# Kernel tuning notes

Hardware: AMD Instinct MI355X
Metric: run time of the kernel (lower is better)

## Reference

```python
import jax, jax.numpy as jnp
import numpy as np

K = 3        # ksize
S = 2        # stride_1
P = K // 2   # padding
SCALE = 10.0 # softmax_scale


def conv1x1(x, w, bias):
    # x: [bs, C, D, H, W], w: [O, C] (1x1x1 Conv3d), bias: [O]
    return jnp.einsum('bcdhw,oc->bodhw', x, w) + bias[None, :, None, None, None]


def _win_idx(n_in):
    n_out = (n_in + 2 * P - K) // S + 1
    idx = (jnp.arange(n_out) * S)[:, None] + jnp.arange(K)  # [n_out, K]
    return idx, n_out


def unfold2d(x):
    # x: [bs, C, H, W] -> patches [bs, C, nH, nW, K, K] (torch Unfold semantics, zero pad)
    bs, C, H, W = x.shape
    xp = jnp.pad(x, ((0, 0), (0, 0), (P, P), (P, P)))
    ri, nH = _win_idx(H)
    ci, nW = _win_idx(W)
    return xp[:, :, ri[:, None, :, None], ci[None, :, None, :]]


def fold2d(pat, H, W):
    # pat: [bs, C, nH, nW, K, K] -> [bs, C, H, W] via overlap-add (torch Fold)
    bs, C, nH, nW, _, _ = pat.shape
    ri, _ = _win_idx(H)
    ci, _ = _win_idx(W)
    out = jnp.zeros((bs, C, H + 2 * P, W + 2 * P), pat.dtype)
    out = out.at[:, :, ri[:, None, :, None], ci[None, :, None, :]].add(pat)
    return out[:, :, P:P + H, P:P + W]


def _patches_flat(x2d):
    # x2d: [bs, Ci, H, W] -> ([bs*L, Ci*K*K], nH, nW)  matching torch's
    # unfold -> view(bs,Ci,K,K,L) -> permute(0,4,1,2,3) -> reshape layout
    pat = unfold2d(x2d)                      # [bs, Ci, nH, nW, K, K]
    bs, Ci, nH, nW = pat.shape[:4]
    flat = jnp.transpose(pat, (0, 2, 3, 1, 4, 5)).reshape(bs * nH * nW, Ci * K * K)
    return flat, nH, nW


def salsa_one(b_one, g_w, g_b, th_w, th_b, ph_w, ph_b, W_w, W_b):
    bs, C, D, H, W = b_one.shape
    Ci = g_w.shape[0]
    b1 = conv1x1(b_one, g_w, g_b)    # query source
    b2 = conv1x1(b_one, th_w, th_b)  # value source
    b3 = conv1x1(b_one, ph_w, ph_b)  # key source
    mid = D // 2

    q, nH, nW = _patches_flat(b1[:, :, mid])   # [bs*L, Ci*K*K]
    v, _, _ = _patches_flat(b2[:, :, mid])
    kq, _, _ = _patches_flat(b3[:, :, mid])

    att = jax.nn.softmax(SCALE * (q @ kq.T), axis=1)  # [bs*L, bs*L]
    zi = att @ v                                      # [bs*L, Ci*K*K]

    pat = jnp.transpose(zi.reshape(bs, nH, nW, Ci, K, K), (0, 3, 1, 2, 4, 5))
    zi2 = fold2d(pat, H, W)                           # [bs, Ci, H, W]
    # overlap-count normalization: fold(unfold(ones))
    mask = fold2d(unfold2d(jnp.ones((bs, Ci, H, W), b_one.dtype)), H, W)
    zi2 = zi2 / mask

    zi5 = jnp.broadcast_to(zi2[:, :, None], (bs, Ci, D, H, W))
    return b_one + conv1x1(zi5, W_w, W_b)


def setup_inputs() -> dict:
    key = jax.random.key(0)
    ks = jax.random.split(key, 9)
    C, Ci = 64, 16
    b = jax.random.normal(ks[0], (2, 1, C, 8, 160, 160), dtype=jnp.float32)
    mk = lambda k, shp: jax.random.normal(k, shp, dtype=jnp.float32) * 0.05
    return {
        'b': b,
        'g_w': mk(ks[1], (Ci, C)), 'g_b': mk(ks[2], (Ci,)),
        'theta_w': mk(ks[3], (Ci, C)), 'theta_b': mk(ks[4], (Ci,)),
        'phi_w': mk(ks[5], (Ci, C)), 'phi_b': mk(ks[6], (Ci,)),
        'W_w': mk(ks[7], (C, Ci)), 'W_b': mk(ks[8], (C,)),
    }


def reference(b, g_w, g_b, theta_w, theta_b, phi_w, phi_b, W_w, W_b):
    f = lambda x: salsa_one(x, g_w, g_b, theta_w, theta_b, phi_w, phi_b, W_w, W_b)
    return jax.vmap(f)(b)
```

## Files before the change

### kernel.cpp

```cpp
#include <hip/hip_runtime.h>


#define NPIX 25600
#define LOG2E10 14.42695040888963f
#define TAU 0.75f

typedef float floatx16 __attribute__((ext_vector_type(16)));
typedef short short8 __attribute__((ext_vector_type(8)));

__device__ inline unsigned short f2bf(float x) {
    union { float f; unsigned int u; } v; v.f = x;
    unsigned int r = v.u + 0x7fffu + ((v.u >> 16) & 1u);
    return (unsigned short)(r >> 16);
}
__device__ inline float bf2f(unsigned short u) {
    union { unsigned int u; float f; } v; v.u = ((unsigned int)u) << 16;
    return v.f;
}

__global__ void k_proj(const float* __restrict__ b,
                       const float* __restrict__ gw, const float* __restrict__ gb,
                       const float* __restrict__ thw, const float* __restrict__ thb,
                       const float* __restrict__ phw, const float* __restrict__ phb,
                       float* __restrict__ P3) {
    __shared__ float Wl[3 * 1024];
    __shared__ float Bl[48];
    int tid = threadIdx.x;
    int g = blockIdx.y;
    int pix = blockIdx.x * 256 + tid;
    for (int i = tid; i < 1024; i += 256) {
        Wl[i]        = gw[i];
        Wl[1024 + i] = phw[i];
        Wl[2048 + i] = thw[i];
    }
    if (tid < 16) { Bl[tid] = gb[tid]; Bl[16 + tid] = phb[tid]; Bl[32 + tid] = thb[tid]; }
    __syncthreads();

    float acc[48];
#pragma unroll
    for (int o = 0; o < 48; o++) acc[o] = 0.f;
    const float* bp = b + (size_t)g * 64 * 8 * NPIX + (size_t)4 * NPIX + pix;
    for (int c = 0; c < 64; c++) {
        float xv = bp[(size_t)c * 8 * NPIX];
#pragma unroll
        for (int o = 0; o < 48; o++)
            acc[o] += Wl[(o >> 4) * 1024 + (o & 15) * 64 + c] * xv;
    }
#pragma unroll
    for (int o = 0; o < 48; o++)
        P3[(size_t)(g * 48 + o) * NPIX + pix] = acc[o] + Bl[o];
}

__global__ void k_unfold_qk(const float* __restrict__ P3, unsigned short* __restrict__ Pat) {
    int idx = blockIdx.x * 256 + threadIdx.x;
    int f = idx % 144;
    int l = (idx / 144) % 6400;
    int s = (idx / (144 * 6400)) & 1;
    int g = idx / (2 * 144 * 6400);
    int ci = f / 9, kr = (f % 9) / 3, kc = f % 3;
    int oh = l / 80, ow = l % 80;
    int h = oh * 2 + kr - 1, w = ow * 2 + kc - 1;
    float v = 0.f;
    if (h >= 0 && h < 160 && w >= 0 && w < 160)
        v = P3[(size_t)(g * 48 + s * 16 + ci) * NPIX + h * 160 + w];
    Pat[idx] = f2bf(v);
}

__global__ void k_unfold_v(const float* __restrict__ P3, unsigned short* __restrict__ VT) {
    int idx = blockIdx.x * 256 + threadIdx.x;
    int l = idx % 6400;
    int f = (idx / 6400) % 144;
    int g = idx / (144 * 6400);
    int ci = f / 9, kr = (f % 9) / 3, kc = f % 3;
    int oh = l / 80, ow = l % 80;
    int h = oh * 2 + kr - 1, w = ow * 2 + kc - 1;
    float v = 0.f;
    if (h >= 0 && h < 160 && w >= 0 && w < 160)
        v = P3[(size_t)(g * 48 + 32 + ci) * NPIX + h * 160 + w];
    VT[idx] = f2bf(v);
}

__global__ __launch_bounds__(256, 2) void k_attn(
    const unsigned short* __restrict__ PatQK, const unsigned short* __restrict__ VT,
    float* __restrict__ ml, unsigned short* __restrict__ Opart,
    int nsplit, int kps) {
    __shared__ unsigned short Ks[64 * 156];
    __shared__ unsigned short Vs[160 * 76];
    __shared__ unsigned short Pl[4 * 32 * 76];

    int tid = threadIdx.x;
    int lane = tid & 63;
    int w = tid >> 6;
    int l31 = lane & 31;
    int h5 = lane >> 5;
    int split = blockIdx.y, g = blockIdx.z;
    int q = blockIdx.x * 128 + w * 32 + l31;
    int nIter = kps >> 6;

    const unsigned short* Qg = PatQK + ((size_t)g * 2 + 0) * 6400 * 144;
    const unsigned short* Kg = PatQK + ((size_t)g * 2 + 1) * 6400 * 144 + (size_t)split * kps * 144;
    const unsigned short* Vg = VT + (size_t)g * 144 * 6400 + split * kps;

    short8 qf[9];
#pragma unroll
    for (int fs = 0; fs < 9; fs++)
        qf[fs] = *(const short8*)(Qg + (size_t)q * 144 + fs * 16 + h5 * 8);

    floatx16 O[5];
#pragma unroll
    for (int i = 0; i < 5; i++) O[i] = (floatx16)0.f;
    float m = -1e30f, lsum = 0.f;

    unsigned short* Plw = Pl + w * (32 * 76);

    short8 stg[9];
    {
#pragma unroll
        for (int j = 0; j < 9; j++) {
            int c = tid + 256 * j;
            if (c < 1152) {
                int row = c / 18, col = c - row * 18;
                stg[j] = *(const short8*)(Kg + row * 144 + col * 8);
            } else {
                int vv = c - 1152;
                int f = vv >> 3, col = vv & 7;
                stg[j] = *(const short8*)(Vg + (size_t)f * 6400 + col * 8);
            }
        }
#pragma unroll
        for (int j = 0; j < 9; j++) {
            int c = tid + 256 * j;
            if (c < 1152) {
                int row = c / 18, col = c - row * 18;
                *(short8*)&Ks[row * 156 + col * 8] = stg[j];
            } else {
                int vv = c - 1152;
                int f = vv >> 3, col = vv & 7;
                *(short8*)&Vs[f * 76 + col * 8] = stg[j];
            }
        }
    }

    for (int it = 0; it < nIter; it++) {
        __syncthreads();

        if (it + 1 < nIter) {
            const unsigned short* Kt = Kg + (it + 1) * 64 * 144;
            const unsigned short* Vt = Vg + (it + 1) * 64;
#pragma unroll
            for (int j = 0; j < 9; j++) {
                int c = tid + 256 * j;
                if (c < 1152) {
                    int row = c / 18, col = c - row * 18;
                    stg[j] = *(const short8*)(Kt + row * 144 + col * 8);
                } else {
                    int vv = c - 1152;
                    int f = vv >> 3, col = vv & 7;
                    stg[j] = *(const short8*)(Vt + (size_t)f * 6400 + col * 8);
                }
            }
        }

        floatx16 S0 = (floatx16)0.f, S1 = (floatx16)0.f;
#pragma unroll
        for (int fs = 0; fs < 9; fs++) {
            short8 a0 = *(const short8*)&Ks[l31 * 156 + fs * 16 + h5 * 8];
            short8 a1 = *(const short8*)&Ks[(32 + l31) * 156 + fs * 16 + h5 * 8];
            S0 = __builtin_amdgcn_mfma_f32_32x32x16_bf16(a0, qf[fs], S0, 0, 0, 0);
            S1 = __builtin_amdgcn_mfma_f32_32x32x16_bf16(a1, qf[fs], S1, 0, 0, 0);
        }

        float mt = -1e30f;
#pragma unroll
        for (int r = 0; r < 16; r++) { mt = fmaxf(mt, S0[r]); mt = fmaxf(mt, S1[r]); }
        mt = fmaxf(mt, __shfl_xor(mt, 32, 64));
        bool upd = mt > m + TAU;
        float mnew = upd ? mt : m;
        float alpha = upd ? exp2f(LOG2E10 * (m - mnew)) : 1.f;
        float ps = 0.f;
#pragma unroll
        for (int r = 0; r < 16; r++) {
            S0[r] = exp2f(LOG2E10 * (S0[r] - mnew));
            S1[r] = exp2f(LOG2E10 * (S1[r] - mnew));
            ps += S0[r] + S1[r];
        }
        ps += __shfl_xor(ps, 32, 64);
        lsum = lsum * alpha + ps;
        m = mnew;
        if (__any(alpha < 1.f)) {
#pragma unroll
            for (int t5 = 0; t5 < 5; t5++)
#pragma unroll
                for (int r = 0; r < 16; r++) O[t5][r] *= alpha;
        }

#pragma unroll
        for (int rg = 0; rg < 4; rg++) {
            ushort4 w0, w1;
            w0.x = f2bf(S0[4 * rg + 0]); w0.y = f2bf(S0[4 * rg + 1]);
            w0.z = f2bf(S0[4 * rg + 2]); w0.w = f2bf(S0[4 * rg + 3]);
            w1.x = f2bf(S1[4 * rg + 0]); w1.y = f2bf(S1[4 * rg + 1]);
            w1.z = f2bf(S1[4 * rg + 2]); w1.w = f2bf(S1[4 * rg + 3]);
            *(ushort4*)&Plw[l31 * 76 + rg * 8 + h5 * 4] = w0;
            *(ushort4*)&Plw[l31 * 76 + 32 + rg * 8 + h5 * 4] = w1;
        }

#pragma unroll
        for (int ks = 0; ks < 4; ks++) {
            short8 pb = *(const short8*)&Plw[l31 * 76 + ks * 16 + h5 * 8];
#pragma unroll
            for (int ft = 0; ft < 5; ft++) {
                short8 va = *(const short8*)&Vs[(ft * 32 + l31) * 76 + ks * 16 + h5 * 8];
                O[ft] = __builtin_amdgcn_mfma_f32_32x32x16_bf16(va, pb, O[ft], 0, 0, 0);
            }
        }

        __syncthreads();
        if (it + 1 < nIter) {
#pragma unroll
            for (int j = 0; j < 9; j++) {
                int c = tid + 256 * j;
                if (c < 1152) {
                    int row = c / 18, col = c - row * 18;
                    *(short8*)&Ks[row * 156 + col * 8] = stg[j];
                } else {
                    int vv = c - 1152;
                    int f = vv >> 3, col = vv & 7;
                    *(short8*)&Vs[f * 76 + col * 8] = stg[j];
                }
            }
        }
    }

    if (h5 == 0)
        ((float2*)ml)[((size_t)g * nsplit + split) * 6400 + q] = make_float2(m, lsum);

    unsigned short* Og = Opart + (((size_t)g * nsplit + split) * 6400 + q) * 144;
#pragma unroll
    for (int ft = 0; ft < 5; ft++)
#pragma unroll
        for (int rg = 0; rg < 4; rg++) {
            int f = ft * 32 + rg * 8 + h5 * 4;
            if (f < 144) {
                ushort4 st;
                st.x = f2bf(O[ft][4 * rg + 0]); st.y = f2bf(O[ft][4 * rg + 1]);
                st.z = f2bf(O[ft][4 * rg + 2]); st.w = f2bf(O[ft][4 * rg + 3]);
                *(ushort4*)(Og + f) = st;
            }
        }
}

__global__ void k_merge(const float* __restrict__ mlp, const unsigned short* __restrict__ Opart,
                        float* __restrict__ Zi, int nsplit) {
    int idx = blockIdx.x * 256 + threadIdx.x;
    int fg = idx % 36;
    int q = (idx / 36) % 6400;
    int g = idx / (36 * 6400);
    const float2* ml2 = (const float2*)mlp;
    float2 s[5];
    float ms = -1e30f;
#pragma unroll
    for (int k = 0; k < 5; k++) {
        s[k] = (k < nsplit) ? ml2[((size_t)g * nsplit + k) * 6400 + q]
                            : make_float2(-1e30f, 0.f);
        ms = fmaxf(ms, s[k].x);
    }
    float wgt[5], denom = 0.f;
#pragma unroll
    for (int k = 0; k < 5; k++) {
        wgt[k] = exp2f(LOG2E10 * (s[k].x - ms));
        denom += wgt[k] * s[k].y;
    }
    float inv = 1.f / denom;
    float a0 = 0.f, a1 = 0.f, a2 = 0.f, a3 = 0.f;
#pragma unroll
    for (int k = 0; k < 5; k++) {
        if (k < nsplit) {
            ushort4 u = *(const ushort4*)(Opart + (((size_t)g * nsplit + k) * 6400 + q) * 144 + fg * 4);
            a0 += wgt[k] * bf2f(u.x); a1 += wgt[k] * bf2f(u.y);
            a2 += wgt[k] * bf2f(u.z); a3 += wgt[k] * bf2f(u.w);
        }
    }
    float4 out = make_float4(a0 * inv, a1 * inv, a2 * inv, a3 * inv);
    *(float4*)(Zi + ((size_t)g * 6400 + q) * 144 + fg * 4) = out;
}

__global__ void k_fold(const float* __restrict__ Zi, float* __restrict__ zi2) {
    int idx = blockIdx.x * 256 + threadIdx.x;
    int pix = idx % NPIX;
    int ci = (idx / NPIX) & 15;
    int g = idx / (16 * NPIX);
    int h = pix / 160, w = pix % 160;
    int ohs[2], krs[2], nh = 0;
#pragma unroll
    for (int kr = 0; kr < 3; kr++) {
        int t = h + 1 - kr;
        if (t >= 0 && (t & 1) == 0 && (t >> 1) < 80) { ohs[nh] = t >> 1; krs[nh] = kr; nh++; }
    }
    int ows[2], kcs[2], nw = 0;
#pragma unroll
    for (int kc = 0; kc < 3; kc++) {
        int t = w + 1 - kc;
        if (t >= 0 && (t & 1) == 0 && (t >> 1) < 80) { ows[nw] = t >> 1; kcs[nw] = kc; nw++; }
    }
    float sm = 0.f;
    for (int a = 0; a < nh; a++)
        for (int bb = 0; bb < nw; bb++) {
            int l = ohs[a] * 80 + ows[bb];
            int f = ci * 9 + krs[a] * 3 + kcs[bb];
            sm += Zi[((size_t)g * 6400 + l) * 144 + f];
        }
    zi2[idx] = sm / (float)(nh * nw);
}

__global__ void k_final(const float* __restrict__ b, const float* __restrict__ zi2,
                        const float* __restrict__ Ww, const float* __restrict__ Wb,
                        float* __restrict__ out) {
    __shared__ float z[16 * 64];
    __shared__ float Wl[64 * 16];
    __shared__ float Bl[64];
    int tid = threadIdx.x;
    int g = blockIdx.y;
    int pxb = blockIdx.x * 64;
    for (int i = tid; i < 1024; i += 256) {
        int ci = i >> 6, px = i & 63;
        z[i] = zi2[(size_t)(g * 16 + ci) * NPIX + pxb + px];
        Wl[i] = Ww[i];
    }
    if (tid < 64) Bl[tid] = Wb[tid];
    __syncthreads();

    int px4 = tid & 15;
    int cg = tid >> 4;
    float acc[4][4];
#pragma unroll
    for (int c4 = 0; c4 < 4; c4++) {
        float bv = Bl[cg + 16 * c4];
#pragma unroll
        for (int j = 0; j < 4; j++) acc[c4][j] = bv;
    }
#pragma unroll
    for (int ci = 0; ci < 16; ci++) {
        float zv[4];
#pragma unroll
        for (int j = 0; j < 4; j++) zv[j] = z[ci * 64 + px4 * 4 + j];
#pragma unroll
        for (int c4 = 0; c4 < 4; c4++) {
            float wv = Wl[(cg + 16 * c4) * 16 + ci];
#pragma unroll
            for (int j = 0; j < 4; j++) acc[c4][j] += wv * zv[j];
        }
    }
    for (int d = 0; d < 8; d++) {
#pragma unroll
        for (int c4 = 0; c4 < 4; c4++) {
            int c = cg + 16 * c4;
            size_t base = ((size_t)(g * 64 + c) * 8 + d) * NPIX + pxb + px4 * 4;
            float4 bv = *(const float4*)(b + base);
            float4 ov = make_float4(bv.x + acc[c4][0], bv.y + acc[c4][1],
                                    bv.z + acc[c4][2], bv.w + acc[c4][3]);
            *(float4*)(out + base) = ov;
        }
    }
}

extern "C" void kernel_launch(void* const* d_in, const int* in_sizes, int n_in,
                              void* d_out, int out_size, void* d_ws, size_t ws_size,
                              hipStream_t stream) {
    const float* b   = (const float*)d_in[0];
    const float* gw  = (const float*)d_in[1];
    const float* gb  = (const float*)d_in[2];
    const float* thw = (const float*)d_in[3];
    const float* thb = (const float*)d_in[4];
    const float* phw = (const float*)d_in[5];
    const float* phb = (const float*)d_in[6];
    const float* Ww  = (const float*)d_in[7];
    const float* Wb  = (const float*)d_in[8];
    float* out = (float*)d_out;
    float* ws = (float*)d_ws;

    const size_t need5 = 30003200;
    int ns = (ws_size >= need5) ? 5 : 4;
    int kps = 6400 / ns;

    unsigned short* PatQK = (unsigned short*)ws;
    unsigned short* VT    = (unsigned short*)(ws + 1843200);
    float*          ml    = ws + 2764800;
    size_t off_P3 = 2764800 + (size_t)2 * ns * 6400 * 2;
    float*          P3    = ws + off_P3;
    unsigned short* Opart = (unsigned short*)(ws + off_P3);
    float*          Zi    = ws;
    float*          zi2   = ws + 1843200;

    k_proj<<<dim3(100, 2), 256, 0, stream>>>(b, gw, gb, thw, thb, phw, phb, P3);
    k_unfold_qk<<<dim3(14400), 256, 0, stream>>>(P3, PatQK);
    k_unfold_v<<<dim3(7200), 256, 0, stream>>>(P3, VT);
    k_attn<<<dim3(50, ns, 2), 256, 0, stream>>>(PatQK, VT, ml, Opart, ns, kps);
    k_merge<<<dim3(1800), 256, 0, stream>>>(ml, Opart, Zi, ns);
    k_fold<<<dim3(3200), 256, 0, stream>>>(Zi, zi2);
    k_final<<<dim3(400, 2), 256, 0, stream>>>(b, zi2, Ww, Wb, out);
}
```

Measured before the change: 399.6 us.

## Keep softmax probabilities in registers and split projection channels across waves

```diff
diff --git a/kernel.cpp b/kernel.cpp
--- a/kernel.cpp
+++ b/kernel.cpp
@@ -7,6 +7,8 @@
 
 typedef float floatx16 __attribute__((ext_vector_type(16)));
 typedef short short8 __attribute__((ext_vector_type(8)));
+
+union U8 { short8 s8; unsigned int u[4]; };
 
 __device__ inline unsigned short f2bf(float x) {
     union { float f; unsigned int u; } v; v.f = x;
@@ -17,21 +19,35 @@
     union { unsigned int u; float f; } v; v.u = ((unsigned int)u) << 16;
     return v.f;
 }
-
-__global__ void k_proj(const float* __restrict__ b,
-                       const float* __restrict__ gw, const float* __restrict__ gb,
-                       const float* __restrict__ thw, const float* __restrict__ thb,
-                       const float* __restrict__ phw, const float* __restrict__ phb,
-                       float* __restrict__ P3) {
-    __shared__ float Wl[3 * 1024];
+__device__ inline unsigned int cvtpk(float a, float b) {
+    unsigned int r;
+    asm("v_cvt_pk_bf16_f32 %0, %1, %2" : "=v"(r) : "v"(a), "v"(b));
+    return r;
+}
+__device__ inline void perm32swap(unsigned int& a, unsigned int& b) {
+    asm("v_permlane32_swap_b32 %0, %1" : "+v"(a), "+v"(b));
+}
+
+__global__ __launch_bounds__(256) void k_proj(
+    const float* __restrict__ b,
+    const float* __restrict__ gw, const float* __restrict__ gb,
+    const float* __restrict__ thw, const float* __restrict__ thb,
+    const float* __restrict__ phw, const float* __restrict__ phb,
+    float* __restrict__ P3) {
+    __shared__ float Wt[3 * 64 * 16];
     __shared__ float Bl[48];
+    __shared__ float red[2][48][64];
     int tid = threadIdx.x;
     int g = blockIdx.y;
-    int pix = blockIdx.x * 256 + tid;
+    int px = tid & 63;
+    int cq = tid >> 6;
+    int pix = blockIdx.x * 64 + px;
+
     for (int i = tid; i < 1024; i += 256) {
-        Wl[i]        = gw[i];
-        Wl[1024 + i] = phw[i];
-        Wl[2048 + i] = thw[i];
+        int o = i & 15, c = i >> 4;
+        Wt[(0 * 64 + c) * 16 + o] = gw[o * 64 + c];
+        Wt[(1 * 64 + c) * 16 + o] = phw[o * 64 + c];
+        Wt[(2 * 64 + c) * 16 + o] = thw[o * 64 + c];
     }
     if (tid < 16) { Bl[tid] = gb[tid]; Bl[16 + tid] = phb[tid]; Bl[32 + tid] = thb[tid]; }
     __syncthreads();
@@ -40,15 +56,38 @@
 #pragma unroll
     for (int o = 0; o < 48; o++) acc[o] = 0.f;
     const float* bp = b + (size_t)g * 64 * 8 * NPIX + (size_t)4 * NPIX + pix;
-    for (int c = 0; c < 64; c++) {
+#pragma unroll
+    for (int i = 0; i < 16; i++) {
+        int c = cq * 16 + i;
         float xv = bp[(size_t)c * 8 * NPIX];
 #pragma unroll
+        for (int s = 0; s < 3; s++) {
+            const float* wp = &Wt[(s * 64 + c) * 16];
+#pragma unroll
+            for (int o = 0; o < 16; o++)
+                acc[s * 16 + o] += wp[o] * xv;
+        }
+    }
+    if (cq >= 2) {
+#pragma unroll
+        for (int o = 0; o < 48; o++) red[cq - 2][o][px] = acc[o];
+    }
+    __syncthreads();
+    if (cq < 2) {
+#pragma unroll
+        for (int o = 0; o < 48; o++) acc[o] += red[cq][o][px];
+    }
+    __syncthreads();
+    if (cq == 1) {
+#pragma unroll
+        for (int o = 0; o < 48; o++) red[0][o][px] = acc[o];
+    }
+    __syncthreads();
+    if (cq == 0) {
+#pragma unroll
         for (int o = 0; o < 48; o++)
-            acc[o] += Wl[(o >> 4) * 1024 + (o & 15) * 64 + c] * xv;
-    }
-#pragma unroll
-    for (int o = 0; o < 48; o++)
-        P3[(size_t)(g * 48 + o) * NPIX + pix] = acc[o] + Bl[o];
+            P3[(size_t)(g * 48 + o) * NPIX + pix] = acc[o] + red[0][o][px] + Bl[o];
+    }
 }
 
 __global__ void k_unfold_qk(const float* __restrict__ P3, unsigned short* __restrict__ Pat) {
@@ -84,9 +123,9 @@
     const unsigned short* __restrict__ PatQK, const unsigned short* __restrict__ VT,
     float* __restrict__ ml, unsigned short* __restrict__ Opart,
     int nsplit, int kps) {
-    __shared__ unsigned short Ks[64 * 156];
-    __shared__ unsigned short Vs[160 * 76];
-    __shared__ unsigned short Pl[4 * 32 * 76];
+    __shared__ unsigned short SM[64 * 156 + 160 * 76];
+    unsigned short* Ks = SM;
+    unsigned short* Vs = SM + 64 * 156;
 
     int tid = threadIdx.x;
     int lane = tid & 63;
@@ -111,57 +150,41 @@
     for (int i = 0; i < 5; i++) O[i] = (floatx16)0.f;
     float m = -1e30f, lsum = 0.f;
 
-    unsigned short* Plw = Pl + w * (32 * 76);
-
+    const unsigned short* gptr[9];
+    int gstep[9], loff[9];
+#pragma unroll
+    for (int j = 0; j < 9; j++) {
+        int c = tid + 256 * j;
+        if (c < 1152) {
+            int row = c / 18, col = c - row * 18;
+            gptr[j] = Kg + row * 144 + col * 8;
+            gstep[j] = 64 * 144;
+            loff[j] = (row * 156 + col * 8) * 2;
+        } else {
+            int vv = c - 1152;
+            int f = vv >> 3, col = vv & 7;
+            gptr[j] = Vg + (size_t)f * 6400 + col * 8;
+            gstep[j] = 64;
+            loff[j] = (64 * 156 + f * 76 + col * 8) * 2;
+        }
+    }
+    char* smb = (char*)SM;
     short8 stg[9];
-    {
-#pragma unroll
-        for (int j = 0; j < 9; j++) {
-            int c = tid + 256 * j;
-            if (c < 1152) {
-                int row = c / 18, col = c - row * 18;
-                stg[j] = *(const short8*)(Kg + row * 144 + col * 8);
-            } else {
-                int vv = c - 1152;
-                int f = vv >> 3, col = vv & 7;
-                stg[j] = *(const short8*)(Vg + (size_t)f * 6400 + col * 8);
-            }
-        }
-#pragma unroll
-        for (int j = 0; j < 9; j++) {
-            int c = tid + 256 * j;
-            if (c < 1152) {
-                int row = c / 18, col = c - row * 18;
-                *(short8*)&Ks[row * 156 + col * 8] = stg[j];
-            } else {
-                int vv = c - 1152;
-                int f = vv >> 3, col = vv & 7;
-                *(short8*)&Vs[f * 76 + col * 8] = stg[j];
-            }
-        }
-    }
+#pragma unroll
+    for (int j = 0; j < 9; j++) { stg[j] = *(const short8*)gptr[j]; gptr[j] += gstep[j]; }
+#pragma unroll
+    for (int j = 0; j < 9; j++) *(short8*)(smb + loff[j]) = stg[j];
 
     for (int it = 0; it < nIter; it++) {
         __syncthreads();
 
         if (it + 1 < nIter) {
-            const unsigned short* Kt = Kg + (it + 1) * 64 * 144;
-            const unsigned short* Vt = Vg + (it + 1) * 64;
-#pragma unroll
-            for (int j = 0; j < 9; j++) {
-                int c = tid + 256 * j;
-                if (c < 1152) {
-                    int row = c / 18, col = c - row * 18;
-                    stg[j] = *(const short8*)(Kt + row * 144 + col * 8);
-                } else {
-                    int vv = c - 1152;
-                    int f = vv >> 3, col = vv & 7;
-                    stg[j] = *(const short8*)(Vt + (size_t)f * 6400 + col * 8);
-                }
-            }
+#pragma unroll
+            for (int j = 0; j < 9; j++) { stg[j] = *(const short8*)gptr[j]; gptr[j] += gstep[j]; }
         }
 
         floatx16 S0 = (floatx16)0.f, S1 = (floatx16)0.f;
+        __builtin_amdgcn_s_setprio(1);
 #pragma unroll
         for (int fs = 0; fs < 9; fs++) {
             short8 a0 = *(const short8*)&Ks[l31 * 156 + fs * 16 + h5 * 8];
@@ -169,21 +192,32 @@
             S0 = __builtin_amdgcn_mfma_f32_32x32x16_bf16(a0, qf[fs], S0, 0, 0, 0);
             S1 = __builtin_amdgcn_mfma_f32_32x32x16_bf16(a1, qf[fs], S1, 0, 0, 0);
         }
-
-        float mt = -1e30f;
-#pragma unroll
-        for (int r = 0; r < 16; r++) { mt = fmaxf(mt, S0[r]); mt = fmaxf(mt, S1[r]); }
+        __builtin_amdgcn_s_setprio(0);
+
+        float mx[8];
+#pragma unroll
+        for (int i = 0; i < 8; i++)
+            mx[i] = fmaxf(fmaxf(S0[2 * i], S0[2 * i + 1]), fmaxf(S1[2 * i], S1[2 * i + 1]));
+        float mt = fmaxf(fmaxf(fmaxf(mx[0], mx[1]), fmaxf(mx[2], mx[3])),
+                         fmaxf(fmaxf(mx[4], mx[5]), fmaxf(mx[6], mx[7])));
         mt = fmaxf(mt, __shfl_xor(mt, 32, 64));
         bool upd = mt > m + TAU;
         float mnew = upd ? mt : m;
         float alpha = upd ? exp2f(LOG2E10 * (m - mnew)) : 1.f;
-        float ps = 0.f;
 #pragma unroll
         for (int r = 0; r < 16; r++) {
             S0[r] = exp2f(LOG2E10 * (S0[r] - mnew));
             S1[r] = exp2f(LOG2E10 * (S1[r] - mnew));
-            ps += S0[r] + S1[r];
-        }
+        }
+        float psa[4] = {0.f, 0.f, 0.f, 0.f};
+#pragma unroll
+        for (int r = 0; r < 16; r += 4) {
+            psa[0] += S0[r] + S1[r];
+            psa[1] += S0[r + 1] + S1[r + 1];
+            psa[2] += S0[r + 2] + S1[r + 2];
+            psa[3] += S0[r + 3] + S1[r + 3];
+        }
+        float ps = (psa[0] + psa[1]) + (psa[2] + psa[3]);
         ps += __shfl_xor(ps, 32, 64);
         lsum = lsum * alpha + ps;
         m = mnew;
@@ -194,41 +228,33 @@
                 for (int r = 0; r < 16; r++) O[t5][r] *= alpha;
         }
 
-#pragma unroll
-        for (int rg = 0; rg < 4; rg++) {
-            ushort4 w0, w1;
-            w0.x = f2bf(S0[4 * rg + 0]); w0.y = f2bf(S0[4 * rg + 1]);
-            w0.z = f2bf(S0[4 * rg + 2]); w0.w = f2bf(S0[4 * rg + 3]);
-            w1.x = f2bf(S1[4 * rg + 0]); w1.y = f2bf(S1[4 * rg + 1]);
-            w1.z = f2bf(S1[4 * rg + 2]); w1.w = f2bf(S1[4 * rg + 3]);
-            *(ushort4*)&Plw[l31 * 76 + rg * 8 + h5 * 4] = w0;
-            *(ushort4*)&Plw[l31 * 76 + 32 + rg * 8 + h5 * 4] = w1;
-        }
-
+        unsigned int P16[16];
+#pragma unroll
+        for (int i = 0; i < 8; i++) P16[i] = cvtpk(S0[2 * i], S0[2 * i + 1]);
+#pragma unroll
+        for (int i = 0; i < 8; i++) P16[8 + i] = cvtpk(S1[2 * i], S1[2 * i + 1]);
+
+        __builtin_amdgcn_s_setprio(1);
 #pragma unroll
         for (int ks = 0; ks < 4; ks++) {
-            short8 pb = *(const short8*)&Plw[l31 * 76 + ks * 16 + h5 * 8];
+            unsigned int a = P16[4 * ks], c2 = P16[4 * ks + 1];
+            unsigned int b2 = P16[4 * ks + 2], d = P16[4 * ks + 3];
+            perm32swap(a, b2);
+            perm32swap(c2, d);
+            U8 pbu;
+            pbu.u[0] = a; pbu.u[1] = c2; pbu.u[2] = b2; pbu.u[3] = d;
 #pragma unroll
             for (int ft = 0; ft < 5; ft++) {
                 short8 va = *(const short8*)&Vs[(ft * 32 + l31) * 76 + ks * 16 + h5 * 8];
-                O[ft] = __builtin_amdgcn_mfma_f32_32x32x16_bf16(va, pb, O[ft], 0, 0, 0);
+                O[ft] = __builtin_amdgcn_mfma_f32_32x32x16_bf16(va, pbu.s8, O[ft], 0, 0, 0);
             }
         }
+        __builtin_amdgcn_s_setprio(0);
 
         __syncthreads();
         if (it + 1 < nIter) {
 #pragma unroll
-            for (int j = 0; j < 9; j++) {
-                int c = tid + 256 * j;
-                if (c < 1152) {
-                    int row = c / 18, col = c - row * 18;
-                    *(short8*)&Ks[row * 156 + col * 8] = stg[j];
-                } else {
-                    int vv = c - 1152;
-                    int f = vv >> 3, col = vv & 7;
-                    *(short8*)&Vs[f * 76 + col * 8] = stg[j];
-                }
-            }
+            for (int j = 0; j < 9; j++) *(short8*)(smb + loff[j]) = stg[j];
         }
     }
 
@@ -242,10 +268,10 @@
         for (int rg = 0; rg < 4; rg++) {
             int f = ft * 32 + rg * 8 + h5 * 4;
             if (f < 144) {
-                ushort4 st;
-                st.x = f2bf(O[ft][4 * rg + 0]); st.y = f2bf(O[ft][4 * rg + 1]);
-                st.z = f2bf(O[ft][4 * rg + 2]); st.w = f2bf(O[ft][4 * rg + 3]);
-                *(ushort4*)(Og + f) = st;
+                uint2 st;
+                st.x = cvtpk(O[ft][4 * rg + 0], O[ft][4 * rg + 1]);
+                st.y = cvtpk(O[ft][4 * rg + 2], O[ft][4 * rg + 3]);
+                *(uint2*)(Og + f) = st;
             }
         }
 }
@@ -392,7 +418,7 @@
     float*          Zi    = ws;
     float*          zi2   = ws + 1843200;
 
-    k_proj<<<dim3(100, 2), 256, 0, stream>>>(b, gw, gb, thw, thb, phw, phb, P3);
+    k_proj<<<dim3(400, 2), 256, 0, stream>>>(b, gw, gb, thw, thb, phw, phb, P3);
     k_unfold_qk<<<dim3(14400), 256, 0, stream>>>(P3, PatQK);
     k_unfold_v<<<dim3(7200), 256, 0, stream>>>(P3, VT);
     k_attn<<<dim3(50, ns, 2), 256, 0, stream>>>(PatQK, VT, ml, Opart, ns, kps);
```

Result: slower. 461.9 us (+15.6%).
